# Kernel tuning notes

Measured on AMD Instinct MI355X. Metric: run time of the kernel, lower is better.

Reference implementation:

```python
import jax, jax.numpy as jnp
import numpy as np
from jax import lax

B, L, E, R = 128, 8, 384, 500
HP, HM, HD = 4, 6, 2   # pair-encoder heads, final-mha heads, dynamic-memory heads
MAXLEN = 8
EPS = 1e-5


def _ln(x, g, b):
    m = x.mean(-1, keepdims=True)
    v = ((x - m) ** 2).mean(-1, keepdims=True)
    return (x - m) / jnp.sqrt(v + EPS) * g + b


def _gelu(x):
    return jax.nn.gelu(x, approximate=False)


def _mha(qi, ki, vi, in_w, in_b, out_w, out_b, h):
    # torch nn.MultiheadAttention with packed in_proj ([3E,E]) and out_proj
    Em = qi.shape[-1]
    dh = Em // h
    q = qi @ in_w[:Em].T + in_b[:Em]
    k = ki @ in_w[Em:2 * Em].T + in_b[Em:2 * Em]
    v = vi @ in_w[2 * Em:].T + in_b[2 * Em:]
    def sp(x):
        b_, l_, _ = x.shape
        return x.reshape(b_, l_, h, dh).transpose(0, 2, 1, 3)
    q, k, v = sp(q), sp(k), sp(v)
    a = jax.nn.softmax(jnp.einsum('bhqd,bhkd->bhqk', q, k) / jnp.sqrt(jnp.float32(dh)), axis=-1)
    o = jnp.einsum('bhqk,bhkd->bhqd', a, v).transpose(0, 2, 1, 3).reshape(qi.shape)
    return o @ out_w.T + out_b


def _forward(inputs, emb, rel_pos, qkv_dyn_w, qkv_dyn_b, out_dyn_w, out_dyn_b,
             ln_dyn_g, ln_dyn_b, conv_w, conv_b, tl_in_w, tl_in_b, tl_out_w, tl_out_b,
             tl_ln1_g, tl_ln1_b, tl_ln2_g, tl_ln2_b, tl_ff1_w, tl_ff1_b, tl_ff2_w, tl_ff2_b,
             fc_score_w, fc_score_b, fcq_w, fcq_b, fck_w, fck_b, fcv_w, fcv_b,
             mha_in_w, mha_in_b, mha_out_w, mha_out_b, lnf1_g, lnf1_b, lnf2_g, lnf2_b,
             ff1_w, ff1_b, ff2_w, ff2_b):
    # ---- update_memory: 2-head self-attention over relation embeddings ----
    rel_emb = emb[:R]                                   # [R,E]
    qkv = rel_emb @ qkv_dyn_w.T + qkv_dyn_b             # [R,3E]
    qm, km, vm = jnp.split(qkv, 3, axis=-1)
    dh = E // HD
    def sph(x):
        return x.reshape(R, HD, dh).transpose(1, 0, 2)  # [HD,R,dh]
    qm, km, vm = sph(qm), sph(km), sph(vm)
    am = jax.nn.softmax(jnp.einsum('hqd,hkd->hqk', qm, km) / jnp.sqrt(jnp.float32(dh)), axis=-1)
    om = jnp.einsum('hqk,hkd->hqd', am, vm).transpose(1, 0, 2).reshape(R, E)
    om = om @ out_dyn_w.T + out_dyn_b
    relation_mem = _ln(rel_emb + om, ln_dyn_g, ln_dyn_b)  # [R,E]

    def pair_encode(x):  # x: [N,2,E]  Conv1d(k=3,pad=1) + 2 post-norm transformer layers
        xc = lax.conv_general_dilated(x.transpose(0, 2, 1), conv_w, (1,), [(1, 1)],
                                      dimension_numbers=('NCH', 'OIH', 'NCH'))
        x = (xc + conv_b[None, :, None]).transpose(0, 2, 1)
        for l in range(2):
            a = _mha(x, x, x, tl_in_w[l], tl_in_b[l], tl_out_w[l], tl_out_b[l], HP)
            x = _ln(x + a, tl_ln1_g[l], tl_ln1_b[l])
            f = _gelu(x @ tl_ff1_w[l].T + tl_ff1_b[l]) @ tl_ff2_w[l].T + tl_ff2_b[l]
            x = _ln(x + f, tl_ln2_g[l], tl_ln2_b[l])
        return x

    def fuse(pair):  # pair: [B,1,E] -> memory_attention_fuse
        mem = jnp.concatenate([jnp.broadcast_to(relation_mem[None], (B, R, E)), pair], axis=1)
        q = pair @ fcq_w.T + fcq_b
        k = mem @ fck_w.T + fck_b
        v = mem @ fcv_w.T + fcv_b
        a = _mha(q, k, v, mha_in_w, mha_in_b, mha_out_w, mha_out_b, HM)
        x = _ln(pair + a, lnf1_g, lnf1_b)
        f = _gelu(x @ ff1_w.T + ff1_b) @ ff2_w.T + ff2_b
        return _ln(x + f, lnf2_g, lnf2_b)

    pos = jnp.minimum(jnp.arange(L), MAXLEN - 1)
    seq = emb[inputs] + rel_pos[pos]                    # [B,L,E]

    losses = []
    for _ in range(L - 1):                              # L-1 sequential reduce steps
        Lc = seq.shape[1]
        if Lc <= 2:
            losses.append(jnp.zeros((B, 1), jnp.float32))
            continue
        # all adjacent pairs at once (replaces the per-pair python loop)
        pairs = jnp.stack([seq[:, :-1], seq[:, 1:]], axis=2) + rel_pos[:2]  # [B,Lc-1,2,E]
        hid = pair_encode(pairs.reshape(B * (Lc - 1), 2, E))[:, -1, :].reshape(B, Lc - 1, E)
        sc = jax.nn.sigmoid(hid @ fc_score_w.T + fc_score_b)[..., 0]        # [B,Lc-1]
        idx = jnp.argmax(sc, axis=-1)                                       # [B]
        logp = jax.nn.log_softmax(sc, axis=-1)
        losses.append(-(jnp.exp(logp) * logp).sum(-1, keepdims=True))       # entropy [B,1]
        sel = jnp.take_along_axis(hid, idx[:, None, None], axis=1)          # [B,1,E]
        fused = fuse(sel)                                                   # [B,1,E]
        # scatter fused at idx, delete row idx+1 (compaction)
        updated = jnp.where(jnp.arange(Lc)[None, :, None] == idx[:, None, None], fused, seq)
        gidx = jnp.arange(Lc - 1)[None, :]
        gidx = gidx + (gidx >= (idx + 1)[:, None])
        seq = jnp.take_along_axis(updated, gidx[:, :, None], axis=1)        # [B,Lc-1,E]

    # ---- final memory_attention ----
    Lf = seq.shape[1]  # == 2
    mem = jnp.concatenate([jnp.broadcast_to(relation_mem[None], (B, R, E)), seq], axis=1)
    q = seq @ fcq_w.T + fcq_b
    k = mem @ fck_w.T + fck_b
    a = _mha(q, k, k, mha_in_w, mha_in_b, mha_out_w, mha_out_b, HM)
    x = _ln(seq + a, lnf1_g, lnf1_b)
    f = _gelu(x @ ff1_w.T + ff1_b) @ ff2_w.T + ff2_b
    x = _ln(x + f, lnf2_g, lnf2_b)
    logits = jnp.einsum('ble,bme->blm', x, mem) / jnp.sqrt(jnp.float32(E))
    gate = jnp.ones((R + Lf,), jnp.float32)             # gate_mask buffer is all ones
    logits = logits * gate                              # [B,Lf,R+Lf]
    logp2 = jax.nn.log_softmax(logits, axis=-1)
    ent = -(jnp.exp(logp2) * logp2).sum(-1)             # [B,Lf]
    loss = jnp.concatenate(losses + [ent], axis=-1)     # [B,L+1]
    pred = logits[:, -1, :]                             # [B,R+Lf]
    return pred, loss


def setup_inputs():
    key = jax.random.key(0)
    ctr = [0]
    def nk():
        ctr[0] += 1
        return jax.random.fold_in(key, ctr[0])
    def W(*s):
        return jax.random.normal(nk(), s, jnp.float32) * 0.02
    def Z(*s):
        return jnp.zeros(s, jnp.float32)
    def O(*s):
        return jnp.ones(s, jnp.float32)
    d = {}
    d['inputs'] = jax.random.randint(nk(), (B, L), 0, R)
    d['emb'] = W(R + 1, E).at[R].set(0.0)  # padding_idx row zero
    d['rel_pos'] = W(MAXLEN, E)
    d['qkv_dyn_w'] = W(3 * E, E); d['qkv_dyn_b'] = Z(3 * E)
    d['out_dyn_w'] = W(E, E); d['out_dyn_b'] = Z(E)
    d['ln_dyn_g'] = O(E); d['ln_dyn_b'] = Z(E)
    d['conv_w'] = W(E, E, 3); d['conv_b'] = Z(E)
    d['tl_in_w'] = W(2, 3 * E, E); d['tl_in_b'] = Z(2, 3 * E)
    d['tl_out_w'] = W(2, E, E); d['tl_out_b'] = Z(2, E)
    d['tl_ln1_g'] = O(2, E); d['tl_ln1_b'] = Z(2, E)
    d['tl_ln2_g'] = O(2, E); d['tl_ln2_b'] = Z(2, E)
    d['tl_ff1_w'] = W(2, 4 * E, E); d['tl_ff1_b'] = Z(2, 4 * E)
    d['tl_ff2_w'] = W(2, E, 4 * E); d['tl_ff2_b'] = Z(2, E)
    d['fc_score_w'] = W(1, E); d['fc_score_b'] = Z(1)
    d['fcq_w'] = W(E, E); d['fcq_b'] = Z(E)
    d['fck_w'] = W(E, E); d['fck_b'] = Z(E)
    d['fcv_w'] = W(E, E); d['fcv_b'] = Z(E)
    d['mha_in_w'] = W(3 * E, E); d['mha_in_b'] = Z(3 * E)
    d['mha_out_w'] = W(E, E); d['mha_out_b'] = Z(E)
    d['lnf1_g'] = O(E); d['lnf1_b'] = Z(E)
    d['lnf2_g'] = O(E); d['lnf2_b'] = Z(E)
    d['ff1_w'] = W(4 * E, E); d['ff1_b'] = Z(4 * E)
    d['ff2_w'] = W(E, 4 * E); d['ff2_b'] = Z(E)
    return d


def reference(inputs, emb, rel_pos, qkv_dyn_w, qkv_dyn_b, out_dyn_w, out_dyn_b,
              ln_dyn_g, ln_dyn_b, conv_w, conv_b, tl_in_w, tl_in_b, tl_out_w, tl_out_b,
              tl_ln1_g, tl_ln1_b, tl_ln2_g, tl_ln2_b, tl_ff1_w, tl_ff1_b, tl_ff2_w, tl_ff2_b,
              fc_score_w, fc_score_b, fcq_w, fcq_b, fck_w, fck_b, fcv_w, fcv_b,
              mha_in_w, mha_in_b, mha_out_w, mha_out_b, lnf1_g, lnf1_b, lnf2_g, lnf2_b,
              ff1_w, ff1_b, ff2_w, ff2_b):
    return _forward(inputs, emb, rel_pos, qkv_dyn_w, qkv_dyn_b, out_dyn_w, out_dyn_b,
                    ln_dyn_g, ln_dyn_b, conv_w, conv_b, tl_in_w, tl_in_b, tl_out_w, tl_out_b,
                    tl_ln1_g, tl_ln1_b, tl_ln2_g, tl_ln2_b, tl_ff1_w, tl_ff1_b, tl_ff2_w, tl_ff2_b,
                    fc_score_w, fc_score_b, fcq_w, fcq_b, fck_w, fck_b, fcv_w, fcv_b,
                    mha_in_w, mha_in_b, mha_out_w, mha_out_b, lnf1_g, lnf1_b, lnf2_g, lnf2_b,
                    ff1_w, ff1_b, ff2_w, ff2_b)
```

## Files before the change

### kernel.cpp

```cpp
#include <hip/hip_runtime.h>

#define CDIV(a,b) (((a)+(b)-1)/(b))

typedef __bf16 bf16x8 __attribute__((ext_vector_type(8)));
typedef float  f32x4  __attribute__((ext_vector_type(4)));
#define MFMA16(a,b,c) __builtin_amdgcn_mfma_f32_16x16x32_bf16(a,b,c,0,0,0)

__device__ __forceinline__ void ldst16(const unsigned short* g, unsigned short* l){
  __builtin_amdgcn_global_load_lds(
      (const __attribute__((address_space(1))) unsigned int*)g,
      (__attribute__((address_space(3))) unsigned int*)l, 16, 0, 0);
}

__device__ __forceinline__ float waveSum(float v){
#pragma unroll
  for(int o=32;o;o>>=1) v += __shfl_xor(v,o);
  return v;
}
__device__ __forceinline__ float waveMax(float v){
#pragma unroll
  for(int o=32;o;o>>=1) v = fmaxf(v,__shfl_xor(v,o));
  return v;
}

// ... 446 lines not shown
#pragma unroll
      for(int mi=0;mi<2;mi++)
#pragma unroll
        for(int ni=0;ni<2;ni++){
          acc[mi][ni] = MFMA16(aH[mi], bH[ni], acc[mi][ni]);
          acc[mi][ni] = MFMA16(aH[mi], bL[ni], acc[mi][ni]);
          acc[mi][ni] = MFMA16(aL[mi], bH[ni], acc[mi][ni]);
        }
    }
  };

  asyncW(kbeg>>6, WsH0, WsL0);
  loadGA(kbeg);
  int k0 = kbeg, kt = kbeg>>6;
  while(true){
    __syncthreads();
    writeLA();
    __syncthreads();
    if(k0+64 < kend){ asyncW(kt+1, WsH1, WsL1); loadGA(k0+64); }
    compute(WsH0, WsL0);
    k0 += 64; kt++;
    if(k0 >= kend) break;
    __syncthreads();
    writeLA();
    __syncthreads();
    if(k0+64 < kend){ asyncW(kt+1, WsH0, WsL0); loadGA(k0+64); }
    compute(WsH1, WsL1);
    k0 += 64; kt++;
    if(k0 >= kend) break;
  }

  float* Cpz = Cp + (size_t)z*M*N;
  const int lr = lane>>4, lc = lane&15;
#pragma unroll
  for(int mi=0;mi<2;mi++)
#pragma unroll
    for(int ni=0;ni<2;ni++)
#pragma unroll
      for(int r=0;r<4;r++){
        int row = bm + wm + mi*16 + lr*4 + r;
        if(row>=M) continue;
        int col = bn + wn + ni*16 + lc;
        Cpz[(size_t)row*N+col] = acc[mi][ni][r];
      }
}

template<int ACT>
__global__ __launch_bounds__(256)
void reduce_k(const float* __restrict__ Cp, float* __restrict__ C,
              const float* __restrict__ bias, int MN, int N, int ldc,
              int sCz, int KS, int NB, float scale)
{
  int gid = blockIdx.x*256+threadIdx.x;
  if(gid >= NB*MN) return;
  int b = gid / MN, e = gid - b*MN;
  int m = e / N, n = e - m*N;
  const float* p = Cp + (size_t)b*KS*MN + e;
  float s = 0.f;
  for(int k=0;k<KS;k++) s += p[(size_t)k*MN];
  s = s*scale + (bias ? bias[n] : 0.f);
  if(ACT==1) s = 0.5f*s*(1.f+erff(s*0.70710678118654752f));
  C[(size_t)b*sCz + (size_t)m*ldc + n] = s;
}

__global__ __launch_bounds__(128)
void reduce_ln(const float* __restrict__ Pp, const float* __restrict__ X,
               float* __restrict__ O, const float* __restrict__ g,
               const float* __restrict__ be, const float* __restrict__ bias,
               int M, int KS)
{
  int row = blockIdx.x;
  if(row>=M) return;
  int tid = threadIdx.x;
  const float* x = X + (size_t)row*384;
  float* o = O + (size_t)row*384;
  float v[3]; float s=0.f;
#pragma unroll
  for(int i=0;i<3;i++){
    int c = tid + i*128;
    float t = bias ? bias[c] : 0.f;
    const float* p = Pp + (size_t)row*384 + c;
    for(int k=0;k<KS;k++) t += p[(size_t)k*M*384];
    v[i] = x[c] + t; s += v[i];
  }
  s = waveSum(s);
  __shared__ float p1[2];
  if((tid&63)==0) p1[tid>>6]=s;
  __syncthreads();
  float mean = (p1[0]+p1[1])*(1.f/384.f);
  float vs=0.f;
#pragma unroll
  for(int i=0;i<3;i++){ float d=v[i]-mean; vs += d*d; }
  vs = waveSum(vs);
  __shared__ float p2[2];
  if((tid&63)==0) p2[tid>>6]=vs;
  __syncthreads();
  float rstd = rsqrtf((p2[0]+p2[1])*(1.f/384.f) + 1e-5f);
#pragma unroll
  for(int i=0;i<3;i++){ int c = tid + i*128; o[c] = (v[i]-mean)*rstd*g[c] + be[c]; }
}

__global__ __launch_bounds__(256)
void gemm_nn(const float* __restrict__ A, int lda,
             const float* __restrict__ Bm, int ldb,
             float* __restrict__ C, int ldc,
             int M, int N, int K, float scale)
{
  __shared__ float As[16][68];
  __shared__ float Bs[16][68];
  const int bm = blockIdx.x*64, bn = blockIdx.y*64;
  const int tid = threadIdx.x;
  const int lr = tid>>2;
  const int kq = (tid&3)<<2;
  const int kr = tid>>4;
  const int nq = (tid&15)<<2;
  const int tx = tid&15, ty = tid>>4;
  float acc[4][4] = {};
  for(int k0=0;k0<K;k0+=16){
    float4 av = make_float4(0.f,0.f,0.f,0.f), bv = make_float4(0.f,0.f,0.f,0.f);
    if(bm+lr < M && k0+kq < K) av = *reinterpret_cast<const float4*>(A + (size_t)(bm+lr)*lda + k0+kq);
    if(k0+kr < K && bn+nq < N) bv = *reinterpret_cast<const float4*>(Bm + (size_t)(k0+kr)*ldb + bn+nq);
    As[kq+0][lr]=av.x; As[kq+1][lr]=av.y; As[kq+2][lr]=av.z; As[kq+3][lr]=av.w;
    Bs[kr][nq+0]=bv.x; Bs[kr][nq+1]=bv.y; Bs[kr][nq+2]=bv.z; Bs[kr][nq+3]=bv.w;
    __syncthreads();
#pragma unroll
    for(int k=0;k<16;k++){
      float4 a4 = *reinterpret_cast<const float4*>(&As[k][ty<<2]);
      float4 b4 = *reinterpret_cast<const float4*>(&Bs[k][tx<<2]);
      float aa[4]={a4.x,a4.y,a4.z,a4.w};
      float bb[4]={b4.x,b4.y,b4.z,b4.w};
#pragma unroll
      for(int i=0;i<4;i++)
#pragma unroll
        for(int j=0;j<4;j++) acc[i][j] = fmaf(aa[i],bb[j],acc[i][j]);
    }
    __syncthreads();
  }
#pragma unroll
  for(int i=0;i<4;i++){
    int row = bm + (ty<<2) + i;
    if(row>=M) continue;
#pragma unroll
    for(int j=0;j<4;j++){
      int col = bn + (tx<<2) + j;
      if(col>=N) continue;
      C[(size_t)row*ldc+col]=acc[i][j]*scale;
    }
  }
}

__global__ __launch_bounds__(128)
void add_ln(const float* __restrict__ X, const float* __restrict__ T,
            float* __restrict__ O, const float* __restrict__ g,
            const float* __restrict__ be, int M)
{
  int row = blockIdx.x;
  if(row>=M) return;
  const float* x = X + (size_t)row*384;
  const float* t = T + (size_t)row*384;
  float* o = O + (size_t)row*384;
  int tid = threadIdx.x;
  float v[3]; float s=0.f;
#pragma unroll
  for(int i=0;i<3;i++){ int c = tid + i*128; v[i] = x[c] + t[c]; s += v[i]; }
  s = waveSum(s);
  __shared__ float p1[2];
  if((tid&63)==0) p1[tid>>6]=s;
  __syncthreads();
  float mean = (p1[0]+p1[1])*(1.f/384.f);
  float vs=0.f;
#pragma unroll
  for(int i=0;i<3;i++){ float d=v[i]-mean; vs += d*d; }
  vs = waveSum(vs);
  __shared__ float p2[2];
  if((tid&63)==0) p2[tid>>6]=vs;
  __syncthreads();
  float rstd = rsqrtf((p2[0]+p2[1])*(1.f/384.f) + 1e-5f);
#pragma unroll
  for(int i=0;i<3;i++){ int c = tid + i*128; o[c] = (v[i]-mean)*rstd*g[c] + be[c]; }
}

__global__ __launch_bounds__(256)
void softmax_rows(float* __restrict__ X, int ld, int cols)
{
  float* x = X + (size_t)blockIdx.x*ld;
  int tid = threadIdx.x;
  float m = -1e30f;
  for(int c=tid;c<cols;c+=256) m = fmaxf(m, x[c]);
  m = waveMax(m);
  __shared__ float sm[4];
  if((tid&63)==0) sm[tid>>6]=m;
  __syncthreads();
  m = fmaxf(fmaxf(sm[0],sm[1]),fmaxf(sm[2],sm[3]));
  float s=0.f;
  for(int c=tid;c<cols;c+=256){ float e = expf(x[c]-m); x[c]=e; s+=e; }
  s = waveSum(s);
  __shared__ float ss[4];
  if((tid&63)==0) ss[tid>>6]=s;
  __syncthreads();
  s = ss[0]+ss[1]+ss[2]+ss[3];
  float inv = 1.f/s;
  for(int c=tid;c<cols;c+=256) x[c]*=inv;
  for(int c=cols+tid;c<ld;c+=256) x[c]=0.f;
}

__global__ void prep_conv(const float* __restrict__ cw, const float* __restrict__ cb,
                          float* __restrict__ Wc, float* __restrict__ cb768){
  int gid = blockIdx.x*256+threadIdx.x;
  if(gid >= 384*384) return;
  int i = gid % 384, o = gid / 384;
  const float* w = cw + (size_t)gid*3;
  Wc[(size_t)o*768 + i]            = w[1];
  Wc[(size_t)o*768 + 384 + i]      = w[2];
  Wc[(size_t)(384+o)*768 + i]      = w[0];
  Wc[(size_t)(384+o)*768 + 384 + i]= w[1];
  if(gid < 768) cb768[gid] = cb[gid % 384];
}

__global__ void vt_k(const float* __restrict__ qkv, float* __restrict__ VT){
  int gid = blockIdx.x*256+threadIdx.x;
  if(gid >= 2*192*512) return;
  int k = gid & 511; int n = (gid>>9) % 192; int h = gid / 98304;
  VT[gid] = (k<500) ? qkv[(size_t)k*1152 + 768 + h*192 + n] : 0.f;
}

__global__ void prep_attn(const float* __restrict__ K1, const float* __restrict__ Vf,
                          const float* __restrict__ Vl, float* __restrict__ Kp,
                          float* __restrict__ VTf, float* __restrict__ VTl){
  int gid = blockIdx.x*256+threadIdx.x;
  if(gid < 196608){
    int j = gid / 384;
    Kp[gid] = (j<500) ? K1[gid] : 0.f;
    return;
  }
  int g2 = gid - 196608;
  const float* V; float* VT;
  if(g2 < 196608){ V = Vf; VT = VTf; }
  else { g2 -= 196608; if(g2 >= 196608) return; V = Vl; VT = VTl; }
  int j = g2 & 511; int d = (g2>>9) & 63; int h = g2 >> 15;
  VT[g2] = (j<500) ? V[(size_t)j*384 + h*64 + d] : 0.f;
}

__global__ void compose_bias(const float* __restrict__ inw, const float* __restrict__ inb,
                             const float* __restrict__ qb, const float* __restrict__ kb,
                             const float* __restrict__ vb, float* __restrict__ cb){
  int gid = blockIdx.x*256+threadIdx.x;
  if(gid>=1536) return;
  int seg = gid/384, i = gid%384;
  const float* wrow; const float* bsrc; float b2;
  if(seg==0){ wrow=inw + (size_t)i*384;       bsrc=qb; b2=inb[i]; }
  else if(seg==1){ wrow=inw + (size_t)(384+i)*384; bsrc=kb; b2=inb[384+i]; }
  else if(seg==2){ wrow=inw + (size_t)(768+i)*384; bsrc=vb; b2=inb[768+i]; }
  else          { wrow=inw + (size_t)(768+i)*384; bsrc=kb; b2=inb[768+i]; }
  float s=0.f;
  for(int t=0;t<384;t++) s = fmaf(wrow[t], bsrc[t], s);
  cb[gid] = s + b2;
}

#define NSEG 18
struct SplitArgs {
  const float* src[NSEG];
  unsigned short* dh[NSEG];
  unsigned short* dl[NSEG];
  int start[NSEG+1];
  int ld[NSEG];
};
__global__ void split_all(SplitArgs a){
  int gid = blockIdx.x*256+threadIdx.x;
  if(gid >= a.start[NSEG]) return;
  int s=0;
  while(s<NSEG-1 && gid >= a.start[s+1]) s++;
  int off = gid - a.start[s];
  int K = a.ld[s];
  int r = off / K, c = off - r*K;
  int dst = ((r>>6)*(K>>6) + (c>>6))*4096 + ((r&63)<<6) + ((c&63) ^ ((r&7)<<3));
  float v = a.src[s][off];
  unsigned short h = f2bf(v);
  a.dh[s][dst] = h;
  a.dl[s][dst] = f2bf(v - bf2f(h));
}

__global__ void seq_init(const int* __restrict__ inp, const float* __restrict__ emb,
                         const float* __restrict__ rp, float* __restrict__ seq){
  int gid = blockIdx.x*256+threadIdx.x;
  if(gid >= 128*8*384) return;
  int j = gid % 384; int l = (gid/384) & 7; int b = gid / 3072;
  int tok = inp[b*8 + l];
  seq[gid] = emb[(size_t)tok*384 + j] + rp[l*384 + j];
}

__global__ void build_pairs(const float* __restrict__ seq, const float* __restrict__ rp,
                            float* __restrict__ pairs, int N, int P){
  int gid = blockIdx.x*256+threadIdx.x;
  if(gid >= N*768) return;
  int c = gid % 768; int n = gid / 768;
  int t = c / 384; int j = c % 384;
  int i = n % P; int b = n / P;
  pairs[gid] = seq[((size_t)b*8 + i + t)*384 + j] + rp[t*384 + j];
}

__global__ __launch_bounds__(256)
void attn2_one(const float* __restrict__ QKV, float* __restrict__ O, int N){
  int n = blockIdx.x;
  if(n>=N) return;
  int tid = threadIdx.x, lane = tid&63, h = tid>>6;
  __shared__ float pr[4][2][2];
  const float* base = QKV + (size_t)(2*n)*1152;
  const float* q0 = base + h*96;
  const float* q1 = base + 1152 + h*96;
  const float* k0 = base + 384 + h*96;
  const float* k1 = base + 1152 + 384 + h*96;
  float q0a=q0[lane], q1a=q1[lane], k0a=k0[lane], k1a=k1[lane];
  float q0b=0.f,q1b=0.f,k0b=0.f,k1b=0.f;
  if(lane<32){ q0b=q0[64+lane]; q1b=q1[64+lane]; k0b=k0[64+lane]; k1b=k1[64+lane]; }
  float s00 = waveSum(q0a*k0a + q0b*k0b);
  float s01 = waveSum(q0a*k1a + q0b*k1b);
  float s10 = waveSum(q1a*k0a + q1b*k0b);
  float s11 = waveSum(q1a*k1a + q1b*k1b);
  if(lane==0){
    const float sc = 0.1020620726159658f;
    s00*=sc; s01*=sc; s10*=sc; s11*=sc;
    float m0=fmaxf(s00,s01); float e00=expf(s00-m0), e01=expf(s01-m0); float i0=1.f/(e00+e01);
    float m1=fmaxf(s10,s11); float e10=expf(s10-m1), e11=expf(s11-m1); float i1=1.f/(e10+e11);
    pr[h][0][0]=e00*i0; pr[h][0][1]=e01*i0;
    pr[h][1][0]=e10*i1; pr[h][1][1]=e11*i1;
  }
  __syncthreads();
  const float* v0 = base + 768;
  const float* v1 = base + 1152 + 768;
  float* o = O + (size_t)(2*n)*384;
#pragma unroll
  for(int i=0;i<3;i++){
    int c = tid + i*256;
    int t = c / 384, j = c % 384; int hh = j/96;
    o[(size_t)t*384 + j] = pr[hh][t][0]*v0[j] + pr[hh][t][1]*v1[j];
  }
}

__global__ void extract_hid(const float* __restrict__ xb, float* __restrict__ hid){
  int gid = blockIdx.x*256+threadIdx.x;
  if(gid >= 128*7*384) return;
  int j = gid % 384; int n = gid / 384;
  hid[gid] = xb[((size_t)(2*n+1))*384 + j];
}

__global__ void scatter_hid(const float* __restrict__ xb, const int* __restrict__ idxb,
                            float* __restrict__ hid, int P){
  int gid = blockIdx.x*256+threadIdx.x;
  if(gid >= 256*384) return;
  int j = gid % 384; int r = gid / 384; int b = r>>1; int e = r&1;
  int s = idxb[b]-1+e; s = max(0, min(s, P-1));
  hid[((size_t)b*7 + s)*384 + j] = xb[((size_t)(2*r+1))*384 + j];
}

__global__ __launch_bounds__(256)
void score_select2(const float* __restrict__ hid, const float* __restrict__ w,
                   const float* __restrict__ b0, int P, int* __restrict__ idxb,
                   float* __restrict__ lossSlot, float* __restrict__ sel){
  int b = blockIdx.x;
  int tid = threadIdx.x, lane = tid&63, wv = tid>>6;
  __shared__ float scs[8];
  __shared__ int sidx;
  for(int pi=wv; pi<P; pi+=4){
    const float* x = hid + ((size_t)b*7 + pi)*384;
    float s=0.f;
#pragma unroll
    for(int i=0;i<6;i++){ int c = lane + i*64; s = fmaf(x[c], w[c], s); }
    s = waveSum(s);
    if(lane==0) scs[pi] = 1.f/(1.f+expf(-(s + b0[0])));
  }
  __syncthreads();
  if(tid==0){
    float m = scs[0]; int am = 0;
    for(int i=1;i<P;i++){ float v=scs[i]; if(v>m){m=v;am=i;} }
    float z=0.f, sx=0.f;
    for(int i=0;i<P;i++){ float e=expf(scs[i]-m); z+=e; sx=fmaf(e,scs[i],sx); }
    lossSlot[(size_t)b*9] = (m + logf(z)) - sx/z;
    idxb[b] = am;
    sidx = am;
  }
  __syncthreads();
  const float* src = hid + ((size_t)b*7 + sidx)*384;
  for(int c=tid;c<384;c+=256) sel[(size_t)b*384+c] = src[c];
}

template<int NE>
__global__ __launch_bounds__(256)
void softmax_ext2(float* __restrict__ S, const float* __restrict__ qkv1,
                  float* __restrict__ E, int R){
  int m = blockIdx.x;
  int r = m % R, h = m / R;
  int rbase = (NE==2) ? (r & ~1) : r;
  float* x = S + (size_t)m*512;
  int tid = threadIdx.x, lane = tid&63, wv = tid>>6;
  __shared__ float r4[4];
  __shared__ float exs[2];
  if(wv < NE){
    const float* q = qkv1 + (size_t)r*1152 + h*64;
    const float* k = qkv1 + (size_t)(rbase+wv)*1152 + 384 + h*64;
    float s = waveSum(q[lane]*k[lane]) * 0.125f;
    if(lane==0) exs[wv] = s;
  }
  __syncthreads();
  float mx = -1e30f;
  for(int c=tid;c<500;c+=256) mx = fmaxf(mx, x[c]);
  if(tid < NE) mx = fmaxf(mx, exs[tid]);
  mx = waveMax(mx);
  if(lane==0) r4[wv]=mx;
  __syncthreads();
  mx = fmaxf(fmaxf(r4[0],r4[1]),fmaxf(r4[2],r4[3]));
  float s=0.f;
  for(int c=tid;c<500;c+=256){ float e=expf(x[c]-mx); x[c]=e; s+=e; }
  float et=0.f;
  if(tid < NE){ et=expf(exs[tid]-mx); s+=et; }
  s = waveSum(s);
  __syncthreads();
  if(lane==0) r4[wv]=s;
  __syncthreads();
  float inv = 1.f/(r4[0]+r4[1]+r4[2]+r4[3]);
  for(int c=tid;c<500;c+=256) x[c]*=inv;
  if(tid < NE) E[(size_t)m*NE+tid] = et*inv;
}

template<int NE>
__global__ void pv_epi2(const float* __restrict__ Pp, const float* __restrict__ E,
                        const float* __restrict__ qkv, float* __restrict__ O, int R){
  int gid = blockIdx.x*256+threadIdx.x;
  if(gid >= R*384) return;
  int r = gid / 384; int c = gid % 384; int h = c >> 6; int d = c & 63;
  int m = h*R + r;
  int rbase = (NE==2) ? (r & ~1) : r;
  const float* p = Pp + ((size_t)(h*8)*R + r)*64 + d;
  float v = 0.f;
#pragma unroll
  for(int k=0;k<8;k++) v += p[(size_t)k*R*64];
#pragma unroll
  for(int e=0;e<NE;e++)
    v = fmaf(E[(size_t)m*NE+e], qkv[(size_t)(rbase+e)*1152 + 768 + c], v);
  O[gid] = v;
}

__global__ void merge_all(const float* __restrict__ seqOld, const float* __restrict__ fused,
                          const float* __restrict__ hidOld, const float* __restrict__ rp,
                          const int* __restrict__ idxb,
                          float* __restrict__ seqNew, float* __restrict__ hidNew,
                          float* __restrict__ pairs, int P, int last){
  int gid = blockIdx.x*256+threadIdx.x;
  int nA = 128*P*384;
  if(gid < nA){
    int j = gid % 384; int rest = gid / 384; int i = rest % P; int b = rest / P;
    int id = idxb[b];
    float v = (i==id) ? fused[(size_t)b*384+j]
                      : seqOld[((size_t)b*8 + i + (i>id?1:0))*384 + j];
    seqNew[((size_t)b*8+i)*384+j] = v;
    return;
  }
  if(last) return;
  gid -= nA;
  int Pn = P-1;
  int nB = 128*Pn*384;
  if(gid < nB){
    int j = gid % 384; int rest = gid / 384; int i = rest % Pn; int b = rest / Pn;
    int idx = idxb[b];
    int si = i + (i>=idx ? 1 : 0);
    hidNew[((size_t)b*7+i)*384+j] = hidOld[((size_t)b*7+si)*384+j];
    return;
  }
  gid -= nB;
  if(gid >= 256*768) return;
  int c = gid % 768; int rr = gid / 768; int b = rr>>1; int e = rr&1;
  int idx = idxb[b];
  int s = idx-1+e; s = max(0, min(s, Pn-1));
  int t = c/384, j = c%384;
  int row = s+t;
  float v = (row==idx) ? fused[(size_t)b*384+j]
                       : seqOld[((size_t)b*8 + row + (row>idx?1:0))*384 + j];
  pairs[gid] = v + rp[t*384+j];
}

__global__ void compact_seq(const float* __restrict__ seq, float* __restrict__ out,
                            float* __restrict__ lossBase){
  int gid = blockIdx.x*256+threadIdx.x;
  if(gid < 128) lossBase[(size_t)gid*9 + 6] = 0.f;
  if(gid >= 256*384) return;
  int j = gid % 384; int r = gid / 384; int b = r>>1; int t = r&1;
  out[gid] = seq[((size_t)b*8 + t)*384 + j];
}

__global__ void logits_k(const float* __restrict__ x2, const float* __restrict__ relmem,
                         const float* __restrict__ seqf, float* __restrict__ out){
  int gid = blockIdx.x*256+threadIdx.x;
  if(gid >= 256*502) return;
  int m = gid % 502; int bt = gid / 502; int b = bt>>1;
  const float* x = x2 + (size_t)bt*384;
  const float* mr = (m<500) ? relmem + (size_t)m*384 : seqf + ((size_t)b*2 + (m-500))*384;
  float s=0.f;
#pragma unroll 8
  for(int d=0;d<384;d++) s = fmaf(x[d], mr[d], s);
  out[gid] = s * 0.05103103630798288f;
}

__global__ void pred_copy(const float* __restrict__ logits, float* __restrict__ out){
  int gid = blockIdx.x*256+threadIdx.x;
  if(gid >= 128*502) return;
  int m = gid % 502; int b = gid / 502;
  out[gid] = logits[((size_t)b*2+1)*502 + m];
}

__global__ __launch_bounds__(256)
void final_ent(const float* __restrict__ L2, float* __restrict__ lossBase){
  int row = blockIdx.x;
  const float* x = L2 + (size_t)row*502;
  int tid = threadIdx.x;
  float m = -1e30f;
  for(int c=tid;c<502;c+=256) m = fmaxf(m, x[c]);
  m = waveMax(m);
  __shared__ float sm[4];
  if((tid&63)==0) sm[tid>>6]=m;
  __syncthreads();
  m = fmaxf(fmaxf(sm[0],sm[1]),fmaxf(sm[2],sm[3]));
  float s=0.f, sx=0.f;
  for(int c=tid;c<502;c+=256){ float e=expf(x[c]-m); s+=e; sx=fmaf(e,x[c],sx); }
  s = waveSum(s); sx = waveSum(sx);
  __shared__ float ps[4], px[4];
  if((tid&63)==0){ ps[tid>>6]=s; px[tid>>6]=sx; }
  __syncthreads();
  if(tid==0){
    float S = ps[0]+ps[1]+ps[2]+ps[3];
    float SX = px[0]+px[1]+px[2]+px[3];
    float ent = (m + logf(S)) - SX/S;
    int b = row>>1, t = row&1;
    lossBase[(size_t)b*9 + 7 + t] = ent;
  }
}

extern "C" void kernel_launch(void* const* d_in, const int* in_sizes, int n_in,
                              void* d_out, int out_size, void* d_ws, size_t ws_size,
                              hipStream_t stream){
  (void)in_sizes; (void)n_in; (void)out_size; (void)ws_size;
  const int*   inputs    = (const int*)  d_in[0];
  const float* emb       = (const float*)d_in[1];
  const float* rel_pos   = (const float*)d_in[2];
  const float* qkv_dyn_w = (const float*)d_in[3];
  const float* qkv_dyn_b = (const float*)d_in[4];
  const float* out_dyn_w = (const float*)d_in[5];
  const float* out_dyn_b = (const float*)d_in[6];
  const float* ln_dyn_g  = (const float*)d_in[7];
  const float* ln_dyn_b  = (const float*)d_in[8];
  const float* conv_w    = (const float*)d_in[9];
  const float* conv_b    = (const float*)d_in[10];
  const float* tl_in_w   = (const float*)d_in[11];
  const float* tl_in_b   = (const float*)d_in[12];
  const float* tl_out_w  = (const float*)d_in[13];
  const float* tl_out_b  = (const float*)d_in[14];
  const float* tl_ln1_g  = (const float*)d_in[15];
  const float* tl_ln1_b  = (const float*)d_in[16];
  const float* tl_ln2_g  = (const float*)d_in[17];
  const float* tl_ln2_b  = (const float*)d_in[18];
  const float* tl_ff1_w  = (const float*)d_in[19];
  const float* tl_ff1_b  = (const float*)d_in[20];
  const float* tl_ff2_w  = (const float*)d_in[21];
  const float* tl_ff2_b  = (const float*)d_in[22];
  const float* fc_score_w= (const float*)d_in[23];
  const float* fc_score_b= (const float*)d_in[24];
  const float* fcq_w     = (const float*)d_in[25];
  const float* fcq_b     = (const float*)d_in[26];
  const float* fck_w     = (const float*)d_in[27];
  const float* fck_b     = (const float*)d_in[28];
  const float* fcv_w     = (const float*)d_in[29];
  const float* fcv_b     = (const float*)d_in[30];
  const float* mha_in_w  = (const float*)d_in[31];
  const float* mha_in_b  = (const float*)d_in[32];
  const float* mha_out_w = (const float*)d_in[33];
  const float* mha_out_b = (const float*)d_in[34];
  const float* lnf1_g    = (const float*)d_in[35];
  const float* lnf1_b    = (const float*)d_in[36];
  const float* lnf2_g    = (const float*)d_in[37];
  const float* lnf2_b    = (const float*)d_in[38];
  const float* ff1_w     = (const float*)d_in[39];
  const float* ff1_b     = (const float*)d_in[40];
  const float* ff2_w     = (const float*)d_in[41];
  const float* ff2_b     = (const float*)d_in[42];

  float* ws = (float*)d_ws;
  size_t off = 0;
  auto Aa = [&](size_t n){ float* p = ws + off; off += n; return p; };
  float* relmem = Aa(192000);
  float* K1mem  = Aa(192000);
  float* V1f    = Aa(192000);
  float* V1l    = Aa(192000);
  float* K1padf = Aa(196608);
  float* VT1f   = Aa(196608);
  float* VT1lf  = Aa(196608);
  float* cb     = Aa(1536);
  float* cb768  = Aa(768);
  float* seqA_  = Aa(393216);
  float* seqB_  = Aa(393216);
  float* hidA_  = Aa(344064);
  float* hidB_  = Aa(344064);
  float* fqkv1  = Aa(147456);
  float* gqkv1  = Aa(294912);
  unsigned short* SH = (unsigned short*)Aa(3514368);
  unsigned short* SL = (unsigned short*)Aa(3514368);
  float* Pp     = Aa(2359296);
  float* pairs  = Aa(688128);
  float* xbuf   = Aa(688128);
  float* qkvbuf = Aa(2064384);
  float* obuf   = Aa(688128);
  float* tmpb   = Aa(688128);
  float* ffbuf  = Aa(2752512);
  float* probs2 = Aa(14336);
  int*   idxb   = (int*)Aa(128);
  float* sel    = Aa(49152);
  float* fo     = Aa(49152);
  float* fxf    = Aa(49152);
  float* ffused = Aa(49152);
  float* fffb   = Aa(196608);

  float* sc512   = ffbuf;
  float* Cfuse3f = ffbuf + 600000;
  float* Cvkf    = ffbuf + 1100000;
  float* Wconvf  = ffbuf + 1300000;
  float* VT      = tmpb;
  float* Sbuf = ffbuf;
  float* Ebuf = probs2;
  float* seqf = pairs;
  float* go   = obuf;
  float* gx1  = obuf + 196608;
  float* gx2  = obuf + 294912;
  float* logitsb = qkvbuf;

  float* lossBase = (float*)d_out + 128*502;

  const int o_qkvdyn=0, o_outdyn=442368, o_wconv=589824,
            o_tlin0=1179648, o_tlin1=1622016, o_tlout0=2064384, o_tlout1=2211840,
            o_tlff1_0=2359296, o_tlff1_1=2949120, o_tlff2_0=3538944, o_tlff2_1=4128768,
            o_mhaout=4718592, o_ff1=4866048, o_ff2=5455872, o_cfuse=6045696, o_cvk=6488064,
            o_vtf=6635520, o_vtl=6832128;
  const int split_total = 7028736;

  const float s192 = 0.07216878364870322f;

  gemm3<0><<<dim3(8,18),256,0,stream>>>(emb,384, qkv_dyn_w,384, qkvbuf,1152, qkv_dyn_b, 500,1152,384, 1.f);
  for(int h=0;h<2;h++)
    gemm3<0><<<dim3(8,8),256,0,stream>>>(qkvbuf + h*192,1152, qkvbuf + 384 + h*192,1152,
           sc512 + (size_t)h*256000,512, nullptr, 500,512,192, s192);
  softmax_rows<<<1000,256,0,stream>>>(sc512, 512, 500);
  vt_k<<<CDIV(2*192*512,256),256,0,stream>>>(qkvbuf, VT);
  for(int h=0;h<2;h++)
    gemm3<0><<<dim3(8,3),256,0,stream>>>(sc512 + (size_t)h*256000,512, VT + h*98304,512,
           obuf + h*192,384, nullptr, 500,192,512, 1.f);
  gemm3<0><<<dim3(8,6),256,0,stream>>>(obuf,384, out_dyn_w,384, xbuf,384, out_dyn_b, 500,384,384, 1.f);
  add_ln<<<500,128,0,stream>>>(emb, xbuf, relmem, ln_dyn_g, ln_dyn_b, 500);

  gemm_nn<<<dim3(6,6),256,0,stream>>>(mha_in_w,384,            fcq_w,384, Cfuse3f,384,          384,384,384, 1.f);
  gemm_nn<<<dim3(6,6),256,0,stream>>>(mha_in_w + 384*384,384,  fck_w,384, Cfuse3f + 147456,384, 384,384,384, 1.f);
  gemm_nn<<<dim3(6,6),256,0,stream>>>(mha_in_w + 768*384,384,  fcv_w,384, Cfuse3f + 294912,384, 384,384,384, 1.f);
  gemm_nn<<<dim3(6,6),256,0,stream>>>(mha_in_w + 768*384,384,  fck_w,384, Cvkf,384,             384,384,384, 1.f);
  compose_bias<<<6,256,0,stream>>>(mha_in_w, mha_in_b, fcq_b, fck_b, fcv_b, cb);

  gemm3<0><<<dim3(8,6),256,0,stream>>>(relmem,384, Cfuse3f + 147456,384, K1mem,384, cb+384,  500,384,384, 1.f);
  gemm3<0><<<dim3(8,6),256,0,stream>>>(relmem,384, Cfuse3f + 294912,384, V1f,384,   cb+768,  500,384,384, 1.f);
  gemm3<0><<<dim3(8,6),256,0,stream>>>(relmem,384, Cvkf,384,            V1l,384,   cb+1152, 500,384,384, 1.f);
  prep_attn<<<CDIV(3*196608,256),256,0,stream>>>(K1mem, V1f, V1l, K1padf, VT1f, VT1lf);

  prep_conv<<<CDIV(384*384,256),256,0,stream>>>(conv_w, conv_b, Wconvf, cb768);

  {
    SplitArgs a;
    const float* srcs[NSEG] = { qkv_dyn_w, out_dyn_w, Wconvf, tl_in_w, tl_in_w + 442368,
                                tl_out_w, tl_out_w + 147456, tl_ff1_w, tl_ff1_w + 589824,
                                tl_ff2_w, tl_ff2_w + 589824, mha_out_w, ff1_w, ff2_w,
                                Cfuse3f, Cvkf, VT1f, VT1lf };
    const int offs[NSEG+1] = { o_qkvdyn, o_outdyn, o_wconv, o_tlin0, o_tlin1, o_tlout0, o_tlout1,
                               o_tlff1_0, o_tlff1_1, o_tlff2_0, o_tlff2_1, o_mhaout, o_ff1, o_ff2,
                               o_cfuse, o_cvk, o_vtf, o_vtl, split_total };
    const int lds[NSEG] = { 384, 384, 768, 384, 384, 384, 384, 384, 384,
                            1536, 1536, 384, 384, 1536, 384, 384, 512, 512 };
    for(int s=0;s<NSEG;s++){
      a.src[s]=srcs[s]; a.dh[s]=SH+offs[s]; a.dl[s]=SL+offs[s]; a.start[s]=offs[s];
      a.ld[s]=lds[s];
    }
    a.start[NSEG]=split_total;
    split_all<<<CDIV(split_total,256),256,0,stream>>>(a);
  }
  seq_init<<<CDIV(128*8*384,256),256,0,stream>>>(inputs, emb, rel_pos, seqA_);

  float* seqCur = seqA_; float* seqNxt = seqB_;
  float* hidCur = hidA_; float* hidNxt = hidB_;

  for(int it=0; it<6; ++it){
    int P = 7 - it;
    if(it == 0){
      int N = 128*7, R2 = 2*N;
      build_pairs<<<CDIV(N*768,256),256,0,stream>>>(seqCur, rel_pos, pairs, N, 7);
      gemm3s<0><<<dim3(N/64,12),256,0,stream>>>(pairs,768, SH+o_wconv,SL+o_wconv,768,
                                                xbuf,768, cb768, N,768,768);
      for(int l=0;l<2;l++){
        int oin  = l? o_tlin1  : o_tlin0;
        int oout = l? o_tlout1 : o_tlout0;
        int of1  = l? o_tlff1_1: o_tlff1_0;
        int of2  = l? o_tlff2_1: o_tlff2_0;
        gemm3s<0><<<dim3(R2/64,18),256,0,stream>>>(xbuf,384, SH+oin,SL+oin,384,
                                                   qkvbuf,1152, tl_in_b + l*1152, R2,1152,384);
        attn2_one<<<N,256,0,stream>>>(qkvbuf, obuf, N);
        gemm3s<0><<<dim3(R2/64,6),256,0,stream>>>(obuf,384, SH+oout,SL+oout,384,
                                                  tmpb,384, tl_out_b + l*384, R2,384,384);
        add_ln<<<R2,128,0,stream>>>(xbuf, tmpb, xbuf, tl_ln1_g + l*384, tl_ln1_b + l*384, R2);
        gemm3s<1><<<dim3(R2/64,24),256,0,stream>>>(xbuf,384, SH+of1,SL+of1,384,
                                                   ffbuf,1536, tl_ff1_b + l*1536, R2,1536,384);
        gemm3s<0><<<dim3(R2/64,6),256,0,stream>>>(ffbuf,1536, SH+of2,SL+of2,1536,
                                                  tmpb,384, tl_ff2_b + l*384, R2,384,1536);
        add_ln<<<R2,128,0,stream>>>(xbuf, tmpb, xbuf, tl_ln2_g + l*384, tl_ln2_b + l*384, R2);
      }
      extract_hid<<<CDIV(128*7*384,256),256,0,stream>>>(xbuf, hidCur);
    } else {
      const int N2 = 256, R2 = 512;
      gemm3bk<<<dim3(4,12,12),256,0,stream>>>(pairs,768,0, SH+o_wconv,SL+o_wconv,768,0,
                                              Pp, N2,768,64,12);
      reduce_k<0><<<CDIV(N2*768,256),256,0,stream>>>(Pp, xbuf, cb768, N2*768,768,768,0,12,1, 1.f);
      for(int l=0;l<2;l++){
        int oin  = l? o_tlin1  : o_tlin0;
        int oout = l? o_tlout1 : o_tlout0;
        int of1  = l? o_tlff1_1: o_tlff1_0;
        int of2  = l? o_tlff2_1: o_tlff2_0;
        gemm3s<0><<<dim3(R2/64,18),256,0,stream>>>(xbuf,384, SH+oin,SL+oin,384,
                                                   qkvbuf,1152, tl_in_b + l*1152, R2,1152,384);
        attn2_one<<<N2,256,0,stream>>>(qkvbuf, obuf, N2);
        gemm3bk<<<dim3(R2/64,6,6),256,0,stream>>>(obuf,384,0, SH+oout,SL+oout,384,0,
                                                  Pp, R2,384,64,6);
        reduce_ln<<<R2,128,0,stream>>>(Pp, xbuf, xbuf, tl_ln1_g + l*384, tl_ln1_b + l*384,
                                       tl_out_b + l*384, R2, 6);
        gemm3s<1><<<dim3(R2/64,24),256,0,stream>>>(xbuf,384, SH+of1,SL+of1,384,
                                                   ffbuf,1536, tl_ff1_b + l*1536, R2,1536,384);
        gemm3bk<<<dim3(R2/64,6,8),256,0,stream>>>(ffbuf,1536,0, SH+of2,SL+of2,1536,0,
                                                  Pp, R2,384,192,8);
        reduce_ln<<<R2,128,0,stream>>>(Pp, xbuf, xbuf, tl_ln2_g + l*384, tl_ln2_b + l*384,
                                       tl_ff2_b + l*384, R2, 8);
      }
      scatter_hid<<<CDIV(256*384,256),256,0,stream>>>(xbuf, idxb, hidCur, P);
    }
    score_select2<<<128,256,0,stream>>>(hidCur, fc_score_w, fc_score_b, P, idxb, lossBase + it, sel);
    gemm3bk<<<dim3(2,18,6),256,0,stream>>>(sel,384,0, SH+o_cfuse,SL+o_cfuse,384,0,
                                           Pp, 128,1152,64,6);
    reduce_k<0><<<CDIV(128*1152,256),256,0,stream>>>(Pp, fqkv1, cb, 128*1152,1152,1152,0,6,1, 1.f);
    gemm3z<<<dim3(2,8,6),256,0,stream>>>(fqkv1,1152,64, K1padf,384,64,
                                         Sbuf,512,128*512, 128,512,64, 0.125f);
    softmax_ext2<1><<<768,256,0,stream>>>(Sbuf, fqkv1, Ebuf, 128);
    gemm3bk<<<dim3(2,1,48),256,0,stream>>>(Sbuf,512,65536, SH+o_vtf,SL+o_vtf,512,32768,
                                           Pp, 128,64,64,8);
    pv_epi2<1><<<CDIV(128*384,256),256,0,stream>>>(Pp, Ebuf, fqkv1, fo, 128);
    gemm3bk<<<dim3(2,6,6),256,0,stream>>>(fo,384,0, SH+o_mhaout,SL+o_mhaout,384,0,
                                          Pp, 128,384,64,6);
    reduce_ln<<<128,128,0,stream>>>(Pp, sel, fxf, lnf1_g, lnf1_b, mha_out_b, 128, 6);
    gemm3bk<<<dim3(2,24,6),256,0,stream>>>(fxf,384,0, SH+o_ff1,SL+o_ff1,384,0,
                                           Pp, 128,1536,64,6);
    reduce_k<1><<<CDIV(128*1536,256),256,0,stream>>>(Pp, fffb, ff1_b, 128*1536,1536,1536,0,6,1, 1.f);
    gemm3bk<<<dim3(2,6,24),256,0,stream>>>(fffb,1536,0, SH+o_ff2,SL+o_ff2,1536,0,
                                           Pp, 128,384,64,24);
    reduce_ln<<<128,128,0,stream>>>(Pp, fxf, ffused, lnf2_g, lnf2_b, ff2_b, 128, 24);
    {
      int last = (it==5) ? 1 : 0;
      int total = 128*P*384 + (last ? 0 : (128*(P-1)*384 + 256*768));
      merge_all<<<CDIV(total,256),256,0,stream>>>(seqCur, ffused, hidCur, rel_pos, idxb,
                                                  seqNxt, hidNxt, pairs, P, last);
    }
    float* t1 = seqCur; seqCur = seqNxt; seqNxt = t1;
    float* t2 = hidCur; hidCur = hidNxt; hidNxt = t2;
  }

  compact_seq<<<CDIV(256*384,256),256,0,stream>>>(seqCur, seqf, lossBase);
  gemm3bk<<<dim3(4,12,6),256,0,stream>>>(seqf,384,0, SH+o_cfuse,SL+o_cfuse,384,0,
                                         Pp, 256,768,64,6);
  reduce_k<0><<<CDIV(256*768,256),256,0,stream>>>(Pp, gqkv1, cb, 256*768,768,1152,0,6,1, 1.f);
  gemm3bk<<<dim3(4,6,6),256,0,stream>>>(seqf,384,0, SH+o_cvk,SL+o_cvk,384,0,
                                        Pp, 256,384,64,6);
  reduce_k<0><<<CDIV(256*384,256),256,0,stream>>>(Pp, gqkv1+768, cb+1152, 256*384,384,1152,0,6,1, 1.f);
  gemm3z<<<dim3(4,8,6),256,0,stream>>>(gqkv1,1152,64, K1padf,384,64,
                                       Sbuf,512,256*512, 256,512,64, 0.125f);
  softmax_ext2<2><<<1536,256,0,stream>>>(Sbuf, gqkv1, Ebuf, 256);
  gemm3bk<<<dim3(4,1,48),256,0,stream>>>(Sbuf,512,131072, SH+o_vtl,SL+o_vtl,512,32768,
                                         Pp, 256,64,64,8);
  pv_epi2<2><<<CDIV(256*384,256),256,0,stream>>>(Pp, Ebuf, gqkv1, go, 256);
  gemm3bk<<<dim3(4,6,6),256,0,stream>>>(go,384,0, SH+o_mhaout,SL+o_mhaout,384,0,
                                        Pp, 256,384,64,6);
  reduce_ln<<<256,128,0,stream>>>(Pp, seqf, gx1, lnf1_g, lnf1_b, mha_out_b, 256, 6);
  gemm3bk<<<dim3(4,24,6),256,0,stream>>>(gx1,384,0, SH+o_ff1,SL+o_ff1,384,0,
                                         Pp, 256,1536,64,6);
  reduce_k<1><<<CDIV(256*1536,256),256,0,stream>>>(Pp, ffbuf, ff1_b, 256*1536,1536,1536,0,6,1, 1.f);
  gemm3bk<<<dim3(4,6,24),256,0,stream>>>(ffbuf,1536,0, SH+o_ff2,SL+o_ff2,1536,0,
                                         Pp, 256,384,64,24);
  reduce_ln<<<256,128,0,stream>>>(Pp, gx1, gx2, lnf2_g, lnf2_b, ff2_b, 256, 24);
  logits_k<<<CDIV(256*502,256),256,0,stream>>>(gx2, relmem, seqf, logitsb);
  pred_copy<<<CDIV(128*502,256),256,0,stream>>>(logitsb, (float*)d_out);
  final_ent<<<256,256,0,stream>>>(logitsb, lossBase);
}
```

Measured before the change: 1.716 ms.

## Fuse hidden-state extract/scatter into LN and scoring; drop split-K for small GEMMs

The extract_hid kernel is folded into the last add_ln, which now also writes odd rows to the hidden buffer. The scatter_hid kernel is folded into a new score_select3 kernel that copies the two fresh pair states before scoring. Several split-K gemm3bk+reduce_k pairs (conv, fused QKV, FF1, final QKV) become single-pass gemm3s launches with fused bias, which removes launches and partial-sum traffic. The tradeoff is fewer blocks per GEMM, so small-M launches may occupy fewer compute units.

Result: slower. 1.768 ms (+3.0%).

```diff
diff --git a/kernel.cpp b/kernel.cpp
--- a/kernel.cpp
+++ b/kernel.cpp
@@ -622,7 +622,7 @@
 __global__ __launch_bounds__(128)
 void add_ln(const float* __restrict__ X, const float* __restrict__ T,
             float* __restrict__ O, const float* __restrict__ g,
-            const float* __restrict__ be, int M)
+            const float* __restrict__ be, int M, float* __restrict__ hid)
 {
   int row = blockIdx.x;
   if(row>=M) return;
@@ -647,7 +647,12 @@
   __syncthreads();
   float rstd = rsqrtf((p2[0]+p2[1])*(1.f/384.f) + 1e-5f);
 #pragma unroll
-  for(int i=0;i<3;i++){ int c = tid + i*128; o[c] = (v[i]-mean)*rstd*g[c] + be[c]; }
+  for(int i=0;i<3;i++){
+    int c = tid + i*128;
+    float r = (v[i]-mean)*rstd*g[c] + be[c];
+    o[c] = r;
+    if(hid && (row&1)) hid[(size_t)(row>>1)*384 + c] = r;
+  }
 }
 
 __global__ __launch_bounds__(256)
@@ -807,30 +812,26 @@
   }
 }
 
-__global__ void extract_hid(const float* __restrict__ xb, float* __restrict__ hid){
-  int gid = blockIdx.x*256+threadIdx.x;
-  if(gid >= 128*7*384) return;
-  int j = gid % 384; int n = gid / 384;
-  hid[gid] = xb[((size_t)(2*n+1))*384 + j];
-}
-
-__global__ void scatter_hid(const float* __restrict__ xb, const int* __restrict__ idxb,
-                            float* __restrict__ hid, int P){
-  int gid = blockIdx.x*256+threadIdx.x;
-  if(gid >= 256*384) return;
-  int j = gid % 384; int r = gid / 384; int b = r>>1; int e = r&1;
-  int s = idxb[b]-1+e; s = max(0, min(s, P-1));
-  hid[((size_t)b*7 + s)*384 + j] = xb[((size_t)(2*r+1))*384 + j];
-}
-
 __global__ __launch_bounds__(256)
-void score_select2(const float* __restrict__ hid, const float* __restrict__ w,
-                   const float* __restrict__ b0, int P, int* __restrict__ idxb,
-                   float* __restrict__ lossSlot, float* __restrict__ sel){
+void score_select3(float* __restrict__ hid, const float* __restrict__ xb,
+                   const float* __restrict__ w, const float* __restrict__ b0,
+                   int P, int* __restrict__ idxb, float* __restrict__ lossSlot,
+                   float* __restrict__ sel, int doScatter){
   int b = blockIdx.x;
   int tid = threadIdx.x, lane = tid&63, wv = tid>>6;
   __shared__ float scs[8];
   __shared__ int sidx;
+  if(doScatter){
+    int oldIdx = idxb[b];
+#pragma unroll
+    for(int e=0;e<2;e++){
+      int s = oldIdx-1+e; s = max(0, min(s, P-1));
+      const float* src = xb + ((size_t)(2*(2*b+e)+1))*384;
+      float* dst = hid + ((size_t)b*7 + s)*384;
+      for(int c=tid;c<384;c+=256) dst[c] = src[c];
+      __syncthreads();
+    }
+  }
   for(int pi=wv; pi<P; pi+=4){
     const float* x = hid + ((size_t)b*7 + pi)*384;
     float s=0.f;
@@ -1121,7 +1122,7 @@
     gemm3<0><<<dim3(8,3),256,0,stream>>>(sc512 + (size_t)h*256000,512, VT + h*98304,512,
            obuf + h*192,384, nullptr, 500,192,512, 1.f);
   gemm3<0><<<dim3(8,6),256,0,stream>>>(obuf,384, out_dyn_w,384, xbuf,384, out_dyn_b, 500,384,384, 1.f);
-  add_ln<<<500,128,0,stream>>>(emb, xbuf, relmem, ln_dyn_g, ln_dyn_b, 500);
+  add_ln<<<500,128,0,stream>>>(emb, xbuf, relmem, ln_dyn_g, ln_dyn_b, 500, nullptr);
 
   gemm_nn<<<dim3(6,6),256,0,stream>>>(mha_in_w,384,            fcq_w,384, Cfuse3f,384,          384,384,384, 1.f);
   gemm_nn<<<dim3(6,6),256,0,stream>>>(mha_in_w + 384*384,384,  fck_w,384, Cfuse3f + 147456,384, 384,384,384, 1.f);
@@ -1176,19 +1177,18 @@
         attn2_one<<<N,256,0,stream>>>(qkvbuf, obuf, N);
         gemm3s<0><<<dim3(R2/64,6),256,0,stream>>>(obuf,384, SH+oout,SL+oout,384,
                                                   tmpb,384, tl_out_b + l*384, R2,384,384);
-        add_ln<<<R2,128,0,stream>>>(xbuf, tmpb, xbuf, tl_ln1_g + l*384, tl_ln1_b + l*384, R2);
+        add_ln<<<R2,128,0,stream>>>(xbuf, tmpb, xbuf, tl_ln1_g + l*384, tl_ln1_b + l*384, R2, nullptr);
         gemm3s<1><<<dim3(R2/64,24),256,0,stream>>>(xbuf,384, SH+of1,SL+of1,384,
                                                    ffbuf,1536, tl_ff1_b + l*1536, R2,1536,384);
         gemm3s<0><<<dim3(R2/64,6),256,0,stream>>>(ffbuf,1536, SH+of2,SL+of2,1536,
                                                   tmpb,384, tl_ff2_b + l*384, R2,384,1536);
-        add_ln<<<R2,128,0,stream>>>(xbuf, tmpb, xbuf, tl_ln2_g + l*384, tl_ln2_b + l*384, R2);
-      }
-      extract_hid<<<CDIV(128*7*384,256),256,0,stream>>>(xbuf, hidCur);
+        add_ln<<<R2,128,0,stream>>>(xbuf, tmpb, xbuf, tl_ln2_g + l*384, tl_ln2_b + l*384, R2,
+                                    (l==1) ? hidCur : nullptr);
+      }
     } else {
       const int N2 = 256, R2 = 512;
-      gemm3bk<<<dim3(4,12,12),256,0,stream>>>(pairs,768,0, SH+o_wconv,SL+o_wconv,768,0,
-                                              Pp, N2,768,64,12);
-      reduce_k<0><<<CDIV(N2*768,256),256,0,stream>>>(Pp, xbuf, cb768, N2*768,768,768,0,12,1, 1.f);
+      gemm3s<0><<<dim3(4,12),256,0,stream>>>(pairs,768, SH+o_wconv,SL+o_wconv,768,
+                                             xbuf,768, cb768, N2,768,768);
       for(int l=0;l<2;l++){
         int oin  = l? o_tlin1  : o_tlin0;
         int oout = l? o_tlout1 : o_tlout0;
@@ -1208,12 +1208,11 @@
         reduce_ln<<<R2,128,0,stream>>>(Pp, xbuf, xbuf, tl_ln2_g + l*384, tl_ln2_b + l*384,
                                        tl_ff2_b + l*384, R2, 8);
       }
-      scatter_hid<<<CDIV(256*384,256),256,0,stream>>>(xbuf, idxb, hidCur, P);
-    }
-    score_select2<<<128,256,0,stream>>>(hidCur, fc_score_w, fc_score_b, P, idxb, lossBase + it, sel);
-    gemm3bk<<<dim3(2,18,6),256,0,stream>>>(sel,384,0, SH+o_cfuse,SL+o_cfuse,384,0,
-                                           Pp, 128,1152,64,6);
-    reduce_k<0><<<CDIV(128*1152,256),256,0,stream>>>(Pp, fqkv1, cb, 128*1152,1152,1152,0,6,1, 1.f);
+    }
+    score_select3<<<128,256,0,stream>>>(hidCur, xbuf, fc_score_w, fc_score_b, P, idxb,
+                                        lossBase + it, sel, (it>0) ? 1 : 0);
+    gemm3s<0><<<dim3(2,18),256,0,stream>>>(sel,384, SH+o_cfuse,SL+o_cfuse,384,
+                                           fqkv1,1152, cb, 128,1152,384);
     gemm3z<<<dim3(2,8,6),256,0,stream>>>(fqkv1,1152,64, K1padf,384,64,
                                          Sbuf,512,128*512, 128,512,64, 0.125f);
     softmax_ext2<1><<<768,256,0,stream>>>(Sbuf, fqkv1, Ebuf, 128);
@@ -1223,9 +1222,8 @@
     gemm3bk<<<dim3(2,6,6),256,0,stream>>>(fo,384,0, SH+o_mhaout,SL+o_mhaout,384,0,
                                           Pp, 128,384,64,6);
     reduce_ln<<<128,128,0,stream>>>(Pp, sel, fxf, lnf1_g, lnf1_b, mha_out_b, 128, 6);
-    gemm3bk<<<dim3(2,24,6),256,0,stream>>>(fxf,384,0, SH+o_ff1,SL+o_ff1,384,0,
-                                           Pp, 128,1536,64,6);
-    reduce_k<1><<<CDIV(128*1536,256),256,0,stream>>>(Pp, fffb, ff1_b, 128*1536,1536,1536,0,6,1, 1.f);
+    gemm3s<1><<<dim3(2,24),256,0,stream>>>(fxf,384, SH+o_ff1,SL+o_ff1,384,
+                                           fffb,1536, ff1_b, 128,1536,384);
     gemm3bk<<<dim3(2,6,24),256,0,stream>>>(fffb,1536,0, SH+o_ff2,SL+o_ff2,1536,0,
                                            Pp, 128,384,64,24);
     reduce_ln<<<128,128,0,stream>>>(Pp, fxf, ffused, lnf2_g, lnf2_b, ff2_b, 128, 24);
@@ -1240,12 +1238,10 @@
   }
 
   compact_seq<<<CDIV(256*384,256),256,0,stream>>>(seqCur, seqf, lossBase);
-  gemm3bk<<<dim3(4,12,6),256,0,stream>>>(seqf,384,0, SH+o_cfuse,SL+o_cfuse,384,0,
-                                         Pp, 256,768,64,6);
-  reduce_k<0><<<CDIV(256*768,256),256,0,stream>>>(Pp, gqkv1, cb, 256*768,768,1152,0,6,1, 1.f);
-  gemm3bk<<<dim3(4,6,6),256,0,stream>>>(seqf,384,0, SH+o_cvk,SL+o_cvk,384,0,
-                                        Pp, 256,384,64,6);
-  reduce_k<0><<<CDIV(256*384,256),256,0,stream>>>(Pp, gqkv1+768, cb+1152, 256*384,384,1152,0,6,1, 1.f);
+  gemm3s<0><<<dim3(4,12),256,0,stream>>>(seqf,384, SH+o_cfuse,SL+o_cfuse,384,
+                                         gqkv1,1152, cb, 256,768,384);
+  gemm3s<0><<<dim3(4,6),256,0,stream>>>(seqf,384, SH+o_cvk,SL+o_cvk,384,
+                                        gqkv1+768,1152, cb+1152, 256,384,384);
   gemm3z<<<dim3(4,8,6),256,0,stream>>>(gqkv1,1152,64, K1padf,384,64,
                                        Sbuf,512,256*512, 256,512,64, 0.125f);
   softmax_ext2<2><<<1536,256,0,stream>>>(Sbuf, gqkv1, Ebuf, 256);
@@ -1255,9 +1251,8 @@
   gemm3bk<<<dim3(4,6,6),256,0,stream>>>(go,384,0, SH+o_mhaout,SL+o_mhaout,384,0,
                                         Pp, 256,384,64,6);
   reduce_ln<<<256,128,0,stream>>>(Pp, seqf, gx1, lnf1_g, lnf1_b, mha_out_b, 256, 6);
-  gemm3bk<<<dim3(4,24,6),256,0,stream>>>(gx1,384,0, SH+o_ff1,SL+o_ff1,384,0,
-                                         Pp, 256,1536,64,6);
-  reduce_k<1><<<CDIV(256*1536,256),256,0,stream>>>(Pp, ffbuf, ff1_b, 256*1536,1536,1536,0,6,1, 1.f);
+  gemm3s<1><<<dim3(4,24),256,0,stream>>>(gx1,384, SH+o_ff1,SL+o_ff1,384,
+                                         ffbuf,1536, ff1_b, 256,1536,384);
   gemm3bk<<<dim3(4,6,24),256,0,stream>>>(ffbuf,1536,0, SH+o_ff2,SL+o_ff2,1536,0,
                                          Pp, 256,384,64,24);
   reduce_ln<<<256,128,0,stream>>>(Pp, gx1, gx2, lnf2_g, lnf2_b, ff2_b, 256, 24);
```
